# Performance work log

Measured on AMD Instinct MI355X. Metric: run time of the kernel, lower is better.

Reference implementation:

```python
import jax, jax.numpy as jnp
import numpy as np

GAMMA = 2.0  # focal focusing parameter
LAM = 0.1    # disco weight


def _centered_dist(x, nw):
    """Doubly (weighted) centered pairwise |x_i - x_j| matrix, as in distance_corr."""
    d = jnp.abs(x[:, None] - x[None, :])          # [N, N]
    davg = jnp.mean(d * nw, axis=1)               # [N]  (row-wise weighted mean)
    return d - davg[None, :] - davg[:, None] + jnp.mean(davg * nw)


def _dcorr(Amat, Bmat, nw):
    ABavg = jnp.mean(Amat * Bmat * nw, axis=1)
    AAavg = jnp.mean(Amat * Amat * nw, axis=1)
    BBavg = jnp.mean(Bmat * Bmat * nw, axis=1)
    return jnp.mean(ABavg * nw) / jnp.sqrt(jnp.mean(AAavg * nw) * jnp.mean(BBavg * nw))


def setup_inputs() -> dict:
    key = jax.random.key(0)
    k1, k2, k3, k4 = jax.random.split(key, 4)
    N, C = 8192, 4
    return {
        "outputs": jax.random.normal(k1, (N, C), dtype=jnp.float32),
        "labels": jax.random.randint(k2, (N,), 0, C, dtype=jnp.int32),
        "event": jax.random.normal(k3, (N,), dtype=jnp.float32),
        "weights": jax.random.uniform(k4, (N, 1), dtype=jnp.float32, minval=0.1, maxval=1.0),
    }


def reference(outputs, labels, event, weights):
    N, C = outputs.shape
    w = weights.squeeze()                          # [N]

    # Focal loss (reduction='none'), alpha=None
    logp = jax.nn.log_softmax(outputs, axis=1)     # [N, C]
    logpt = logp[jnp.arange(N), labels]            # [N]
    pt = jnp.exp(logpt)
    focal = -(1.0 - pt) ** GAMMA * logpt * w       # per-example, times weights

    probs = jnp.exp(logp)                          # softmax(outputs)
    nw = w * N / jnp.sum(w)                        # normed weights (sum == N)

    # event-side centered distance matrix is class-independent: compute once
    Bmat = _centered_dist(event, nw)               # [N, N]

    disco = jnp.float32(0.0)
    for i in range(C):                             # small fixed class loop
        Amat = _centered_dist(probs[:, i], nw)
        disco = disco + _dcorr(Amat, Bmat, nw)
    disco = disco / C

    f = jnp.mean(focal)
    return jnp.stack([f, disco, f + LAM * disco])  # [focal, disco, tot]
```

## Files before the change

kernel.cpp:

```cpp
#include <hip/hip_runtime.h>
#include <math.h>

#define BLK 256
#define IT 4
#define JSPLIT 128
#define LAM 0.1f


__device__ __forceinline__ float wave_reduce(float v) {
    v += __shfl_down(v, 32, 64);
    v += __shfl_down(v, 16, 64);
    v += __shfl_down(v, 8, 64);
    v += __shfl_down(v, 4, 64);
    v += __shfl_down(v, 2, 64);
    v += __shfl_down(v, 1, 64);
    return v;
}

__global__ __launch_bounds__(BLK) void k1_rowprep(
        const float* __restrict__ outs, const int* __restrict__ labels,
        const float* __restrict__ event, const float* __restrict__ wts,
        float* __restrict__ probs, float* __restrict__ rows,
        float* __restrict__ scal, float* __restrict__ kpart, int N) {
    __shared__ float red[4][12];
    int i = blockIdx.x * BLK + threadIdx.x;
    float4 o = ((const float4*)outs)[i];
    float m = fmaxf(fmaxf(o.x, o.y), fmaxf(o.z, o.w));
    float e0 = expf(o.x - m), e1 = expf(o.y - m), e2 = expf(o.z - m), e3 = expf(o.w - m);
    float s = e0 + e1 + e2 + e3;
    float inv = 1.0f / s;
    float4 p = make_float4(e0 * inv, e1 * inv, e2 * inv, e3 * inv);
    ((float4*)probs)[i] = p;

    int l = labels[i];
    float ol = (l == 0) ? o.x : (l == 1) ? o.y : (l == 2) ? o.z : o.w;
    float logpt = ol - m - logf(s);
    float pt = expf(logpt);
    float w = wts[i];
    float ev = event[i];
    float om = 1.0f - pt;
    float focal = -om * om * logpt * w;

#pragma unroll
    for (int v = 0; v < 5; ++v) rows[v * N + i] = 0.f;
    if (blockIdx.x == 0 && threadIdx.x < 16) scal[threadIdx.x] = 0.f;

    float vals[12] = {focal, w,
                      w * p.x, w * p.y, w * p.z, w * p.w, w * ev,
                      w * p.x * p.x, w * p.y * p.y, w * p.z * p.z,
                      w * p.w * p.w, w * ev * ev};
    int lane = threadIdx.x & 63, wave = threadIdx.x >> 6;
#pragma unroll
    for (int k = 0; k < 12; ++k) {
        float r = wave_reduce(vals[k]);
        if (lane == 0) red[wave][k] = r;
    }
    __syncthreads();
    if (threadIdx.x < 12)
        kpart[blockIdx.x * 12 + threadIdx.x] =
            red[0][threadIdx.x] + red[1][threadIdx.x] + red[2][threadIdx.x] + red[3][threadIdx.x];
}

__global__ __launch_bounds__(BLK) void k2_pairs(
        const float4* __restrict__ probs4, const float* __restrict__ event,
        const float* __restrict__ wts, float* __restrict__ rows,
        float* __restrict__ scal, int N) {
    __shared__ float4 jp[64];
    __shared__ float2 jew[64];
    __shared__ float red[4][4];

    int tid = threadIdx.x;
    int itile = blockIdx.x;
    int jsp = blockIdx.y;
    int jcount = N / JSPLIT;
    int jbase = jsp * jcount;
    int ibase = itile * (BLK * IT) + tid;

    float4 pi[IT];
    float ei[IT], wi[IT];
#pragma unroll
    for (int k = 0; k < IT; ++k) {
        int i = ibase + k * BLK;
        pi[k] = probs4[i];
        ei[k] = event[i];
        wi[k] = wts[i];
    }

    if (tid < 64) {
        int j = jbase + tid;
        jp[tid] = probs4[j];
        jew[tid] = make_float2(event[j], wts[j]);
    }
    __syncthreads();

    float s[IT][5], t[IT][4];
#pragma unroll
    for (int k = 0; k < IT; ++k) {
#pragma unroll
        for (int v = 0; v < 5; ++v) s[k][v] = 0.f;
#pragma unroll
        for (int v = 0; v < 4; ++v) t[k][v] = 0.f;
    }

#pragma unroll 8
    for (int jj = 0; jj < 64; ++jj) {
        float4 p = jp[jj];
        float2 ew = jew[jj];
        float wj = ew.y;
#pragma unroll
        for (int k = 0; k < IT; ++k) {
            float d0 = pi[k].x - p.x;
            float d1 = pi[k].y - p.y;
            float d2 = pi[k].z - p.z;
            float d3 = pi[k].w - p.w;
            float de = ei[k] - ew.x;
            s[k][0] = fmaf(wj, fabsf(d0), s[k][0]);
            s[k][1] = fmaf(wj, fabsf(d1), s[k][1]);
            s[k][2] = fmaf(wj, fabsf(d2), s[k][2]);
            s[k][3] = fmaf(wj, fabsf(d3), s[k][3]);
            float wde = wj * fabsf(de);
            s[k][4] += wde;
            t[k][0] = fmaf(wde, fabsf(d0), t[k][0]);
            t[k][1] = fmaf(wde, fabsf(d1), t[k][1]);
            t[k][2] = fmaf(wde, fabsf(d2), t[k][2]);
            t[k][3] = fmaf(wde, fabsf(d3), t[k][3]);
        }
    }

#pragma unroll
    for (int k = 0; k < IT; ++k) {
        int i = ibase + k * BLK;
        atomicAdd(&rows[0 * N + i], s[k][0]);
        atomicAdd(&rows[1 * N + i], s[k][1]);
        atomicAdd(&rows[2 * N + i], s[k][2]);
        atomicAdd(&rows[3 * N + i], s[k][3]);
        atomicAdd(&rows[4 * N + i], s[k][4]);
    }

    float tc0 = t[0][0] * wi[0] + t[1][0] * wi[1] + t[2][0] * wi[2] + t[3][0] * wi[3];
    float tc1 = t[0][1] * wi[0] + t[1][1] * wi[1] + t[2][1] * wi[2] + t[3][1] * wi[3];
    float tc2 = t[0][2] * wi[0] + t[1][2] * wi[1] + t[2][2] * wi[2] + t[3][2] * wi[3];
    float tc3 = t[0][3] * wi[0] + t[1][3] * wi[1] + t[2][3] * wi[2] + t[3][3] * wi[3];
    int lane = tid & 63, wave = tid >> 6;
    tc0 = wave_reduce(tc0); tc1 = wave_reduce(tc1);
    tc2 = wave_reduce(tc2); tc3 = wave_reduce(tc3);
    if (lane == 0) {
        red[wave][0] = tc0; red[wave][1] = tc1;
        red[wave][2] = tc2; red[wave][3] = tc3;
    }
    __syncthreads();
    if (tid < 4)
        atomicAdd(&scal[tid], red[0][tid] + red[1][tid] + red[2][tid] + red[3][tid]);
}

__global__ __launch_bounds__(1024) void k3_final(
        const float* __restrict__ rows, const float* __restrict__ scal,
        const float* __restrict__ wts, const float* __restrict__ kpart,
        float* __restrict__ out, int N) {
    __shared__ float red[16][14];
    __shared__ float fin[12];
    int tid = threadIdx.x, lane = tid & 63, wave = tid >> 6;

    if (wave == 0) {
#pragma unroll
        for (int k = 0; k < 12; ++k) {
            float v = (lane < 32) ? kpart[lane * 12 + k] : 0.f;
            v = wave_reduce(v);
            if (lane == 0) fin[k] = v;
        }
    }

    float acc[14];
#pragma unroll
    for (int k = 0; k < 14; ++k) acc[k] = 0.f;

    for (int i = tid; i < N; i += 1024) {
        float w = wts[i];
        float s0 = rows[0 * N + i], s1 = rows[1 * N + i], s2 = rows[2 * N + i],
              s3 = rows[3 * N + i], sE = rows[4 * N + i];
        acc[0] += w * s0; acc[1] += w * s1; acc[2] += w * s2;
        acc[3] += w * s3; acc[4] += w * sE;
        float wE = w * sE;
        acc[5] += wE * s0; acc[6] += wE * s1; acc[7] += wE * s2; acc[8] += wE * s3;
        acc[9] += wE * sE;
        acc[10] += w * s0 * s0; acc[11] += w * s1 * s1;
        acc[12] += w * s2 * s2; acc[13] += w * s3 * s3;
    }

#pragma unroll
    for (int k = 0; k < 14; ++k) acc[k] = wave_reduce(acc[k]);
    if (lane == 0) {
#pragma unroll
        for (int k = 0; k < 14; ++k) red[wave][k] = acc[k];
    }
    __syncthreads();

    if (tid == 0) {
        float SW[5], SWW_ce[4], SWW_ee, SWW_cc[4];
#pragma unroll
        for (int k = 0; k < 5; ++k) {
            float a = 0.f;
            for (int wv = 0; wv < 16; ++wv) a += red[wv][k];
            SW[k] = a;
        }
#pragma unroll
        for (int k = 0; k < 4; ++k) {
            float a = 0.f;
            for (int wv = 0; wv < 16; ++wv) a += red[wv][5 + k];
            SWW_ce[k] = a;
        }
        {
            float a = 0.f;
            for (int wv = 0; wv < 16; ++wv) a += red[wv][9];
            SWW_ee = a;
        }
#pragma unroll
        for (int k = 0; k < 4; ++k) {
            float a = 0.f;
            for (int wv = 0; wv < 16; ++wv) a += red[wv][10 + k];
            SWW_cc[k] = a;
        }

        float focal_sum = fin[0];
        float W = fin[1];
        float M1[5] = {fin[2], fin[3], fin[4], fin[5], fin[6]};
        float M2[5] = {fin[7], fin[8], fin[9], fin[10], fin[11]};

        float invW2 = 1.0f / (W * W);
        float invW3 = invW2 / W;

        float g[5];
#pragma unroll
        for (int v = 0; v < 5; ++v) g[v] = SW[v] * invW2;
        float gE = g[4];

        float Tee = 2.0f * (W * M2[4] - M1[4] * M1[4]);
        float num_ee = Tee * invW2 - 2.0f * SWW_ee * invW3 + gE * gE;

        float disco = 0.f;
#pragma unroll
        for (int c = 0; c < 4; ++c) {
            float Tcc = 2.0f * (W * M2[c] - M1[c] * M1[c]);
            float num_cc = Tcc * invW2 - 2.0f * SWW_cc[c] * invW3 + g[c] * g[c];
            float num_ce = scal[c] * invW2 - 2.0f * SWW_ce[c] * invW3 + g[c] * gE;
            disco += num_ce * rsqrtf(num_cc * num_ee);
        }
        disco *= 0.25f;

        float f = focal_sum / (float)N;
        out[0] = f;
        out[1] = disco;
        out[2] = f + LAM * disco;
    }
}

extern "C" void kernel_launch(void* const* d_in, const int* in_sizes, int n_in,
                              void* d_out, int out_size, void* d_ws, size_t ws_size,
                              hipStream_t stream) {
    const float* outs = (const float*)d_in[0];
    const int* labels = (const int*)d_in[1];
    const float* event = (const float*)d_in[2];
    const float* wts = (const float*)d_in[3];
    float* out = (float*)d_out;
    int N = in_sizes[1];

    float* ws = (float*)d_ws;
    float* probs = ws;
    float* rows = probs + (size_t)N * 4;
    float* scal = rows + (size_t)N * 5;
    float* kpart = scal + 16;

    k1_rowprep<<<N / BLK, BLK, 0, stream>>>(outs, labels, event, wts, probs,
                                            rows, scal, kpart, N);

    dim3 g2(N / (BLK * IT), JSPLIT);
    k2_pairs<<<g2, BLK, 0, stream>>>((const float4*)probs, event, wts, rows, scal, N);

    k3_final<<<1, 1024, 0, stream>>>(rows, scal, wts, kpart, out, N);
}
```

Before: 108.7 us.

## Fuse softmax prep into pair kernel, replace row atomics with partial buffers

Removes the separate row-prep kernel by recomputing softmax probabilities inside the pair kernel for both the i and j tiles. The jsp==0 blocks also compute the focal and moment partials. Per-row atomics are replaced by plain stores into per-split partial buffers, and the single-block final kernel becomes a 64-block reduction that finishes with a last-block-done pattern. This cuts one launch, the zeroing pass and the atomic contention, at the cost of redundant exp work and a larger partial buffer (5*128*N floats) that kB must read back. scalB[18] doubles as the arrival counter: it is zeroed in kA and reinterpreted as an unsigned int in kB.

```diff
diff --git a/kernel.cpp b/kernel.cpp
--- a/kernel.cpp
+++ b/kernel.cpp
@@ -4,6 +4,9 @@
 #define BLK 256
 #define IT 4
 #define JSPLIT 128
+#define NITILE 8
+#define BBLK 128
+#define BGRID 64
 #define LAM 0.1f
 
 
@@ -17,79 +20,87 @@
     return v;
 }
 
-__global__ __launch_bounds__(BLK) void k1_rowprep(
+__global__ __launch_bounds__(BLK) void kA(
         const float* __restrict__ outs, const int* __restrict__ labels,
         const float* __restrict__ event, const float* __restrict__ wts,
-        float* __restrict__ probs, float* __restrict__ rows,
-        float* __restrict__ scal, float* __restrict__ kpart, int N) {
-    __shared__ float red[4][12];
-    int i = blockIdx.x * BLK + threadIdx.x;
-    float4 o = ((const float4*)outs)[i];
-    float m = fmaxf(fmaxf(o.x, o.y), fmaxf(o.z, o.w));
-    float e0 = expf(o.x - m), e1 = expf(o.y - m), e2 = expf(o.z - m), e3 = expf(o.w - m);
-    float s = e0 + e1 + e2 + e3;
-    float inv = 1.0f / s;
-    float4 p = make_float4(e0 * inv, e1 * inv, e2 * inv, e3 * inv);
-    ((float4*)probs)[i] = p;
-
-    int l = labels[i];
-    float ol = (l == 0) ? o.x : (l == 1) ? o.y : (l == 2) ? o.z : o.w;
-    float logpt = ol - m - logf(s);
-    float pt = expf(logpt);
-    float w = wts[i];
-    float ev = event[i];
-    float om = 1.0f - pt;
-    float focal = -om * om * logpt * w;
-
-#pragma unroll
-    for (int v = 0; v < 5; ++v) rows[v * N + i] = 0.f;
-    if (blockIdx.x == 0 && threadIdx.x < 16) scal[threadIdx.x] = 0.f;
-
-    float vals[12] = {focal, w,
-                      w * p.x, w * p.y, w * p.z, w * p.w, w * ev,
-                      w * p.x * p.x, w * p.y * p.y, w * p.z * p.z,
-                      w * p.w * p.w, w * ev * ev};
-    int lane = threadIdx.x & 63, wave = threadIdx.x >> 6;
-#pragma unroll
-    for (int k = 0; k < 12; ++k) {
-        float r = wave_reduce(vals[k]);
-        if (lane == 0) red[wave][k] = r;
-    }
-    __syncthreads();
-    if (threadIdx.x < 12)
-        kpart[blockIdx.x * 12 + threadIdx.x] =
-            red[0][threadIdx.x] + red[1][threadIdx.x] + red[2][threadIdx.x] + red[3][threadIdx.x];
-}
-
-__global__ __launch_bounds__(BLK) void k2_pairs(
-        const float4* __restrict__ probs4, const float* __restrict__ event,
-        const float* __restrict__ wts, float* __restrict__ rows,
-        float* __restrict__ scal, int N) {
+        float* __restrict__ rowsP, float* __restrict__ tceP,
+        float* __restrict__ momP, float* __restrict__ scalB, int N) {
     __shared__ float4 jp[64];
     __shared__ float2 jew[64];
-    __shared__ float red[4][4];
+    __shared__ float red4[4][4];
+    __shared__ float red12[4][12];
 
     int tid = threadIdx.x;
     int itile = blockIdx.x;
     int jsp = blockIdx.y;
-    int jcount = N / JSPLIT;
-    int jbase = jsp * jcount;
     int ibase = itile * (BLK * IT) + tid;
+
+    if (itile == 0 && jsp == 0 && tid < 20) scalB[tid] = 0.f;
+
+    if (tid < 64) {
+        int j = jsp * 64 + tid;
+        float4 o = ((const float4*)outs)[j];
+        float m = fmaxf(fmaxf(o.x, o.y), fmaxf(o.z, o.w));
+        float e0 = expf(o.x - m), e1 = expf(o.y - m),
+              e2 = expf(o.z - m), e3 = expf(o.w - m);
+        float inv = 1.0f / (e0 + e1 + e2 + e3);
+        jp[tid] = make_float4(e0 * inv, e1 * inv, e2 * inv, e3 * inv);
+        jew[tid] = make_float2(event[j], wts[j]);
+    }
 
     float4 pi[IT];
     float ei[IT], wi[IT];
 #pragma unroll
     for (int k = 0; k < IT; ++k) {
         int i = ibase + k * BLK;
-        pi[k] = probs4[i];
+        float4 o = ((const float4*)outs)[i];
+        float m = fmaxf(fmaxf(o.x, o.y), fmaxf(o.z, o.w));
+        float e0 = expf(o.x - m), e1 = expf(o.y - m),
+              e2 = expf(o.z - m), e3 = expf(o.w - m);
+        float inv = 1.0f / (e0 + e1 + e2 + e3);
+        pi[k] = make_float4(e0 * inv, e1 * inv, e2 * inv, e3 * inv);
         ei[k] = event[i];
         wi[k] = wts[i];
     }
 
-    if (tid < 64) {
-        int j = jbase + tid;
-        jp[tid] = probs4[j];
-        jew[tid] = make_float2(event[j], wts[j]);
+    if (jsp == 0) {
+        float acc12[12];
+#pragma unroll
+        for (int k = 0; k < 12; ++k) acc12[k] = 0.f;
+#pragma unroll
+        for (int k = 0; k < IT; ++k) {
+            int i = ibase + k * BLK;
+            float4 o = ((const float4*)outs)[i];
+            float m = fmaxf(fmaxf(o.x, o.y), fmaxf(o.z, o.w));
+            float e0 = expf(o.x - m), e1 = expf(o.y - m),
+                  e2 = expf(o.z - m), e3 = expf(o.w - m);
+            float s = e0 + e1 + e2 + e3;
+            int l = labels[i];
+            float ol = (l == 0) ? o.x : (l == 1) ? o.y : (l == 2) ? o.z : o.w;
+            float logpt = ol - m - logf(s);
+            float pt = expf(logpt);
+            float om = 1.0f - pt;
+            float w = wi[k], ev = ei[k];
+            float4 p = pi[k];
+            acc12[0] += -om * om * logpt * w;
+            acc12[1] += w;
+            acc12[2] += w * p.x;  acc12[3] += w * p.y;
+            acc12[4] += w * p.z;  acc12[5] += w * p.w;
+            acc12[6] += w * ev;
+            acc12[7] += w * p.x * p.x;  acc12[8] += w * p.y * p.y;
+            acc12[9] += w * p.z * p.z;  acc12[10] += w * p.w * p.w;
+            acc12[11] += w * ev * ev;
+        }
+        int lane = tid & 63, wave = tid >> 6;
+#pragma unroll
+        for (int k = 0; k < 12; ++k) {
+            float r = wave_reduce(acc12[k]);
+            if (lane == 0) red12[wave][k] = r;
+        }
+        __syncthreads();
+        if (tid < 12)
+            momP[itile * 12 + tid] =
+                red12[0][tid] + red12[1][tid] + red12[2][tid] + red12[3][tid];
     }
     __syncthreads();
 
@@ -130,11 +141,9 @@
 #pragma unroll
     for (int k = 0; k < IT; ++k) {
         int i = ibase + k * BLK;
-        atomicAdd(&rows[0 * N + i], s[k][0]);
-        atomicAdd(&rows[1 * N + i], s[k][1]);
-        atomicAdd(&rows[2 * N + i], s[k][2]);
-        atomicAdd(&rows[3 * N + i], s[k][3]);
-        atomicAdd(&rows[4 * N + i], s[k][4]);
+#pragma unroll
+        for (int v = 0; v < 5; ++v)
+            rowsP[(v * JSPLIT + jsp) * N + i] = s[k][v];
     }
 
     float tc0 = t[0][0] * wi[0] + t[1][0] * wi[1] + t[2][0] * wi[2] + t[3][0] * wi[3];
@@ -145,81 +154,86 @@
     tc0 = wave_reduce(tc0); tc1 = wave_reduce(tc1);
     tc2 = wave_reduce(tc2); tc3 = wave_reduce(tc3);
     if (lane == 0) {
-        red[wave][0] = tc0; red[wave][1] = tc1;
-        red[wave][2] = tc2; red[wave][3] = tc3;
+        red4[wave][0] = tc0; red4[wave][1] = tc1;
+        red4[wave][2] = tc2; red4[wave][3] = tc3;
     }
     __syncthreads();
     if (tid < 4)
-        atomicAdd(&scal[tid], red[0][tid] + red[1][tid] + red[2][tid] + red[3][tid]);
-}
-
-__global__ __launch_bounds__(1024) void k3_final(
-        const float* __restrict__ rows, const float* __restrict__ scal,
-        const float* __restrict__ wts, const float* __restrict__ kpart,
-        float* __restrict__ out, int N) {
-    __shared__ float red[16][14];
+        tceP[(jsp * NITILE + itile) * 4 + tid] =
+            red4[0][tid] + red4[1][tid] + red4[2][tid] + red4[3][tid];
+}
+
+__global__ __launch_bounds__(BBLK) void kB(
+        const float* __restrict__ rowsP, const float* __restrict__ tceP,
+        const float* __restrict__ momP, const float* __restrict__ wts,
+        float* __restrict__ scalB, float* __restrict__ out, int N) {
+    __shared__ float red[2][14];
     __shared__ float fin[12];
-    int tid = threadIdx.x, lane = tid & 63, wave = tid >> 6;
-
-    if (wave == 0) {
-#pragma unroll
-        for (int k = 0; k < 12; ++k) {
-            float v = (lane < 32) ? kpart[lane * 12 + k] : 0.f;
-            v = wave_reduce(v);
-            if (lane == 0) fin[k] = v;
-        }
-    }
-
-    float acc[14];
-#pragma unroll
-    for (int k = 0; k < 14; ++k) acc[k] = 0.f;
-
-    for (int i = tid; i < N; i += 1024) {
-        float w = wts[i];
-        float s0 = rows[0 * N + i], s1 = rows[1 * N + i], s2 = rows[2 * N + i],
-              s3 = rows[3 * N + i], sE = rows[4 * N + i];
-        acc[0] += w * s0; acc[1] += w * s1; acc[2] += w * s2;
-        acc[3] += w * s3; acc[4] += w * sE;
-        float wE = w * sE;
-        acc[5] += wE * s0; acc[6] += wE * s1; acc[7] += wE * s2; acc[8] += wE * s3;
-        acc[9] += wE * sE;
-        acc[10] += w * s0 * s0; acc[11] += w * s1 * s1;
-        acc[12] += w * s2 * s2; acc[13] += w * s3 * s3;
-    }
-
-#pragma unroll
-    for (int k = 0; k < 14; ++k) acc[k] = wave_reduce(acc[k]);
-    if (lane == 0) {
-#pragma unroll
-        for (int k = 0; k < 14; ++k) red[wave][k] = acc[k];
-    }
-    __syncthreads();
-
+    __shared__ float sc[18];
+    __shared__ unsigned int last;
+
+    int tid = threadIdx.x;
+    int i = blockIdx.x * BBLK + tid;
+
+    float s0 = 0.f, s1 = 0.f, s2 = 0.f, s3 = 0.f, sE = 0.f;
+#pragma unroll 8
+    for (int jsp = 0; jsp < JSPLIT; ++jsp) {
+        s0 += rowsP[(0 * JSPLIT + jsp) * N + i];
+        s1 += rowsP[(1 * JSPLIT + jsp) * N + i];
+        s2 += rowsP[(2 * JSPLIT + jsp) * N + i];
+        s3 += rowsP[(3 * JSPLIT + jsp) * N + i];
+        sE += rowsP[(4 * JSPLIT + jsp) * N + i];
+    }
+
+    float w = wts[i];
+    float a[14];
+    a[0] = w * s0; a[1] = w * s1; a[2] = w * s2; a[3] = w * s3; a[4] = w * sE;
+    float wE = w * sE;
+    a[5] = wE * s0; a[6] = wE * s1; a[7] = wE * s2; a[8] = wE * s3; a[9] = wE * sE;
+    a[10] = w * s0 * s0; a[11] = w * s1 * s1;
+    a[12] = w * s2 * s2; a[13] = w * s3 * s3;
+
+    int lane = tid & 63, wave = tid >> 6;
+#pragma unroll
+    for (int k = 0; k < 14; ++k) {
+        float r = wave_reduce(a[k]);
+        if (lane == 0) red[wave][k] = r;
+    }
+    __syncthreads();
+    if (tid < 14) atomicAdd(&scalB[tid], red[0][tid] + red[1][tid]);
+
+    if (tid < 64) {
+        float v = tceP[(blockIdx.x * 16 + (tid >> 2)) * 4 + (tid & 3)];
+        v += __shfl_down(v, 32, 64);
+        v += __shfl_down(v, 16, 64);
+        v += __shfl_down(v, 8, 64);
+        v += __shfl_down(v, 4, 64);
+        if (tid < 4) atomicAdd(&scalB[14 + tid], v);
+    }
+
+    __syncthreads();
     if (tid == 0) {
-        float SW[5], SWW_ce[4], SWW_ee, SWW_cc[4];
-#pragma unroll
-        for (int k = 0; k < 5; ++k) {
-            float a = 0.f;
-            for (int wv = 0; wv < 16; ++wv) a += red[wv][k];
-            SW[k] = a;
-        }
-#pragma unroll
-        for (int k = 0; k < 4; ++k) {
-            float a = 0.f;
-            for (int wv = 0; wv < 16; ++wv) a += red[wv][5 + k];
-            SWW_ce[k] = a;
-        }
-        {
-            float a = 0.f;
-            for (int wv = 0; wv < 16; ++wv) a += red[wv][9];
-            SWW_ee = a;
-        }
-#pragma unroll
-        for (int k = 0; k < 4; ++k) {
-            float a = 0.f;
-            for (int wv = 0; wv < 16; ++wv) a += red[wv][10 + k];
-            SWW_cc[k] = a;
-        }
+        __threadfence();
+        last = atomicAdd((unsigned int*)&scalB[18], 1u);
+    }
+    __syncthreads();
+    if (last != BGRID - 1) return;
+
+    __threadfence();
+    if (tid < 12) {
+        float aa = 0.f;
+#pragma unroll
+        for (int tI = 0; tI < NITILE; ++tI) aa += momP[tI * 12 + tid];
+        fin[tid] = aa;
+    }
+    if (tid < 18) sc[tid] = atomicAdd(&scalB[tid], 0.0f);
+    __syncthreads();
+
+    if (tid == 0) {
+        float SW[5]     = {sc[0], sc[1], sc[2], sc[3], sc[4]};
+        float SWW_ce[4] = {sc[5], sc[6], sc[7], sc[8]};
+        float SWW_ee    = sc[9];
+        float SWW_cc[4] = {sc[10], sc[11], sc[12], sc[13]};
 
         float focal_sum = fin[0];
         float W = fin[1];
@@ -242,7 +256,7 @@
         for (int c = 0; c < 4; ++c) {
             float Tcc = 2.0f * (W * M2[c] - M1[c] * M1[c]);
             float num_cc = Tcc * invW2 - 2.0f * SWW_cc[c] * invW3 + g[c] * g[c];
-            float num_ce = scal[c] * invW2 - 2.0f * SWW_ce[c] * invW3 + g[c] * gE;
+            float num_ce = sc[14 + c] * invW2 - 2.0f * SWW_ce[c] * invW3 + g[c] * gE;
             disco += num_ce * rsqrtf(num_cc * num_ee);
         }
         disco *= 0.25f;
@@ -265,16 +279,12 @@
     int N = in_sizes[1];
 
     float* ws = (float*)d_ws;
-    float* probs = ws;
-    float* rows = probs + (size_t)N * 4;
-    float* scal = rows + (size_t)N * 5;
-    float* kpart = scal + 16;
-
-    k1_rowprep<<<N / BLK, BLK, 0, stream>>>(outs, labels, event, wts, probs,
-                                            rows, scal, kpart, N);
-
-    dim3 g2(N / (BLK * IT), JSPLIT);
-    k2_pairs<<<g2, BLK, 0, stream>>>((const float4*)probs, event, wts, rows, scal, N);
-
-    k3_final<<<1, 1024, 0, stream>>>(rows, scal, wts, kpart, out, N);
-}
+    float* rowsP = ws;
+    float* tceP = rowsP + (size_t)5 * JSPLIT * N;
+    float* momP = tceP + (size_t)NITILE * JSPLIT * 4;
+    float* scalB = momP + NITILE * 12;
+
+    dim3 gA(N / (BLK * IT), JSPLIT);
+    kA<<<gA, BLK, 0, stream>>>(outs, labels, event, wts, rowsP, tceP, momP, scalB, N);
+    kB<<<BGRID, BBLK, 0, stream>>>(rowsP, tceP, momP, wts, scalB, out, N);
+}
```

New measurement: 109.0 us. Within noise of the previous version (+0.2%).
